# Performance work log

Hardware: AMD Instinct MI355X
Metric: run time of the kernel (lower is better)

Reference implementation:

```python
import jax, jax.numpy as jnp
import numpy as np

DIM = 256
NUM_HEADS = 4
HEAD_DIM = DIM // NUM_HEADS
EPS = 1e-5


def setup_inputs() -> dict:
    key = jax.random.key(0)
    ks = jax.random.split(key, 8)
    B, N, C = 8, 2048, DIM
    s = 0.02
    return {
        "x": jax.random.normal(ks[0], (B, N, C), jnp.float32),
        "qkv_w": jax.random.normal(ks[1], (C, 3 * C), jnp.float32) * s,
        "qkv_b": jnp.zeros((3 * C,), jnp.float32),
        "proj_w": jax.random.normal(ks[2], (C, C), jnp.float32) * s,
        "proj_b": jnp.zeros((C,), jnp.float32),
        "ln1_g": jnp.ones((C,), jnp.float32),
        "ln1_b": jnp.zeros((C,), jnp.float32),
        "ln2_g": jnp.ones((C,), jnp.float32),
        "ln2_b": jnp.zeros((C,), jnp.float32),
        "mlp_w1": jax.random.normal(ks[3], (C, 2 * C), jnp.float32) * s,
        "mlp_b1": jnp.zeros((2 * C,), jnp.float32),
        "mlp_w2": jax.random.normal(ks[4], (2 * C, C), jnp.float32) * s,
        "mlp_b2": jnp.zeros((C,), jnp.float32),
    }


def _layernorm(x, g, b):
    mu = jnp.mean(x, axis=-1, keepdims=True)
    var = jnp.mean(jnp.square(x - mu), axis=-1, keepdims=True)
    return (x - mu) * jax.lax.rsqrt(var + EPS) * g + b


def reference(x, qkv_w, qkv_b, proj_w, proj_b, ln1_g, ln1_b, ln2_g, ln2_b,
              mlp_w1, mlp_b1, mlp_w2, mlp_b2):
    B, N, C = x.shape
    H, D = NUM_HEADS, HEAD_DIM
    shortcut = x
    h = _layernorm(x, ln1_g, ln1_b)
    qkv = (h @ qkv_w + qkv_b).reshape(B, N, 3, H, D)
    q = qkv[:, :, 0].transpose(0, 2, 1, 3)  # [B,H,N,D]
    k = qkv[:, :, 1].transpose(0, 2, 1, 3)
    v = qkv[:, :, 2].transpose(0, 2, 1, 3)
    attn = jnp.einsum('bhnd,bhmd->bhnm', q, k) * (D ** -0.5)
    attn = jax.nn.softmax(attn, axis=-1)  # dropout = identity (eval mode)
    o = jnp.einsum('bhnm,bhmd->bhnd', attn, v)
    o = o.transpose(0, 2, 1, 3).reshape(B, N, C)
    x = o @ proj_w + proj_b + shortcut
    h2 = _layernorm(x, ln2_g, ln2_b)
    mlp = jax.nn.gelu(h2 @ mlp_w1 + mlp_b1, approximate=False) @ mlp_w2 + mlp_b2
    return x + mlp
```

## Files before the change

kernel.cpp:

```cpp
#include <hip/hip_runtime.h>

typedef __bf16 bf16;
typedef __bf16 bf16x8 __attribute__((ext_vector_type(8)));
typedef __bf16 bf16x4 __attribute__((ext_vector_type(4)));
typedef float  f32x4  __attribute__((ext_vector_type(4)));
typedef unsigned u32x2 __attribute__((ext_vector_type(2)));

typedef __attribute__((address_space(1))) const void GASV;
typedef __attribute__((address_space(3))) void LASV;

__device__ __forceinline__ void gload16(const void* g, void* l) {
  __builtin_amdgcn_global_load_lds((GASV*)g, (LASV*)l, 16, 0, 0);
}

constexpr float CEXP = 0.125f * 1.44269504088896340736f;

__global__ __launch_bounds__(256) void prep_fused(const float* __restrict__ qkv_w,
                                                  const float* __restrict__ proj_w,
                                                  const float* __restrict__ w1,
                                                  const float* __restrict__ w2,
                                                  bf16* __restrict__ Wtqkv,
                                                  bf16* __restrict__ WtP,
                                                  bf16* __restrict__ Wt1,
                                                  bf16* __restrict__ Wt2,
                                                  const float* __restrict__ x,
                                                  const float* __restrict__ gam,
                                                  const float* __restrict__ bet,
                                                  bf16* __restrict__ hout) {
  __shared__ float td[32][33];
  const int blk = blockIdx.x;
  const int tid = threadIdx.x;
  if (blk >= 512) {
    const int lane = tid & 63;
    const int w = tid >> 6;
    const size_t row = (size_t)(blk - 512) * 4 + w;
    const float4 v = *(const float4*)(x + row * 256 + lane * 4);
    float s1 = v.x + v.y + v.z + v.w;
    float s2 = v.x * v.x + v.y * v.y + v.z * v.z + v.w * v.w;
#pragma unroll
    for (int m = 1; m < 64; m <<= 1) {
      s1 += __shfl_xor(s1, m);
      s2 += __shfl_xor(s2, m);
    }
    const float mu = s1 * (1.0f / 256.0f);
    const float var = s2 * (1.0f / 256.0f) - mu * mu;
    const float rs = rsqrtf(var + 1e-5f);
    const float4 g4 = *(const float4*)(gam + lane * 4);
    const float4 b4 = *(const float4*)(bet + lane * 4);
    bf16x4 o;
    o[0] = (bf16)((v.x - mu) * rs * g4.x + b4.x);
    o[1] = (bf16)((v.y - mu) * rs * g4.y + b4.y);
    o[2] = (bf16)((v.z - mu) * rs * g4.z + b4.z);
    o[3] = (bf16)((v.w - mu) * rs * g4.w + b4.w);
    *(bf16x4*)(hout + row * 256 + lane * 4) = o;
    return;
  }
  const int t = blk;
  const float* src;
  bf16* dst;
  int Kin, Nin, kt, nt;
  if (t < 192)      { src = qkv_w; dst = Wtqkv; Kin = 256; Nin = 768; kt = t & 7;          nt = t >> 3; }
  else if (t < 256) { src = proj_w; dst = WtP;  Kin = 256; Nin = 256; kt = (t - 192) & 7;  nt = (t - 192) >> 3; }
  else if (t < 384) { src = w1;    dst = Wt1;   Kin = 256; Nin = 512; kt = (t - 256) & 7;  nt = (t - 256) >> 3; }
  else              { src = w2;    dst = Wt2;   Kin = 512; Nin = 256; kt = (t - 384) & 15; nt = (t - 384) >> 4; }
  {
    const int r = tid >> 3, c4 = (tid & 7) << 2;
    const float4 v = *(const float4*)(src + (size_t)(kt * 32 + r) * Nin + nt * 32 + c4);
    td[r][c4 + 0] = v.x; td[r][c4 + 1] = v.y; td[r][c4 + 2] = v.z; td[r][c4 + 3] = v.w;
  }
  __syncthreads();
  {
    const int n = tid >> 3, k4 = (tid & 7) << 2;
    bf16x4 o;
#pragma unroll
    for (int i = 0; i < 4; ++i) o[i] = (bf16)td[k4 + i][n];
    *(bf16x4*)(dst + (size_t)(nt * 32 + n) * Kin + kt * 32 + k4) = o;
  }
}

__global__ __launch_bounds__(256) void ln_fwd(const float* __restrict__ x,
                                              const float* __restrict__ gam,
                                              const float* __restrict__ bet,
                                              bf16* __restrict__ out) {
  const int lane = threadIdx.x & 63;
  const int w = threadIdx.x >> 6;
  const size_t row = (size_t)blockIdx.x * 4 + w;
  const float4 v = *(const float4*)(x + row * 256 + lane * 4);
  float s1 = v.x + v.y + v.z + v.w;
  float s2 = v.x * v.x + v.y * v.y + v.z * v.z + v.w * v.w;
#pragma unroll
  for (int m = 1; m < 64; m <<= 1) {
    s1 += __shfl_xor(s1, m);
    s2 += __shfl_xor(s2, m);
  }
  const float mu = s1 * (1.0f / 256.0f);
  const float var = s2 * (1.0f / 256.0f) - mu * mu;
  const float rs = rsqrtf(var + 1e-5f);
  const float4 g4 = *(const float4*)(gam + lane * 4);
  const float4 b4 = *(const float4*)(bet + lane * 4);
  bf16x4 o;
  o[0] = (bf16)((v.x - mu) * rs * g4.x + b4.x);
  o[1] = (bf16)((v.y - mu) * rs * g4.y + b4.y);
  o[2] = (bf16)((v.z - mu) * rs * g4.z + b4.z);
  o[3] = (bf16)((v.w - mu) * rs * g4.w + b4.w);
  *(bf16x4*)(out + row * 256 + lane * 4) = o;
}

template <int EPI>
__global__ __launch_bounds__(512) void gemm_bt(const bf16* __restrict__ A,
                                               const bf16* __restrict__ Bt,
                                               const float* __restrict__ bias,
                                               const float* __restrict__ res,
                                               void* __restrict__ outp,
                                               int M, int N, int K) {
  __shared__ bf16 Al[2][8192];
  __shared__ bf16 Bl[2][8192];
  const int tid = threadIdx.x;
  const int lane = tid & 63;
  const int W = tid >> 6;
  const int wm = W >> 2, wn = W & 3;
  const int qi = lane & 15, g = lane >> 4;
  const int nbm = M >> 7;
  const int bm = (int)blockIdx.x % nbm;
  const int bn = (int)blockIdx.x / nbm;
  const int m0 = bm << 7, n0 = bn << 7;
  const int nk = K >> 6;

  const char* asrc[2];
  const char* bsrc[2];
#pragma unroll
  for (int p = 0; p < 2; ++p) {
    const int s = p * 8 + W;
    const int row = (s >> 3) * 64 + ((s >> 1) & 3) * 16 + qi;
    const int kb = (s & 1) * 64 + g * 16;
    asrc[p] = (const char*)(A + (size_t)(m0 + row) * K) + kb;
    bsrc[p] = (const char*)(Bt + (size_t)(n0 + row) * K) + kb;
  }

  f32x4 acc[4][2];
#pragma unroll
  for (int i = 0; i < 4; ++i)
#pragma unroll
    for (int j = 0; j < 2; ++j) acc[i][j] = (f32x4){0.f, 0.f, 0.f, 0.f};

  auto stage = [&](int sl) {
#pragma unroll
    for (int p = 0; p < 2; ++p) {
      gload16(asrc[p], (char*)&Al[sl][0] + (p * 8 + W) * 1024);
      gload16(bsrc[p], (char*)&Bl[sl][0] + (p * 8 + W) * 1024);
      asrc[p] += 128;
      bsrc[p] += 128;
    }
  };

  stage(0);
  asm volatile("s_waitcnt vmcnt(0)" ::: "memory");
  __builtin_amdgcn_s_barrier();

  for (int t = 0; t < nk; ++t) {
    if (t + 1 < nk) stage((t + 1) & 1);
    const char* pa = (const char*)&Al[t & 1][0] + wm * 8192 + lane * 16;
    const char* pb = (const char*)&Bl[t & 1][0] + lane * 16;
    bf16x8 av[4][2], bv[2][2];
#pragma unroll
    for (int f = 0; f < 4; ++f)
#pragma unroll
      for (int ks = 0; ks < 2; ++ks)
        av[f][ks] = *(const bf16x8*)(pa + (f * 2 + ks) * 1024);
#pragma unroll
    for (int fn = 0; fn < 2; ++fn)
#pragma unroll
      for (int ks = 0; ks < 2; ++ks) {
        const int r16 = wn * 2 + fn;
        bv[fn][ks] = *(const bf16x8*)(pb + ((r16 >> 2) * 8 + (r16 & 3) * 2 + ks) * 1024);
      }
    __builtin_amdgcn_s_setprio(1);
#pragma unroll
    for (int fm = 0; fm < 4; ++fm)
#pragma unroll
      for (int fn = 0; fn < 2; ++fn) {
        acc[fm][fn] = __builtin_amdgcn_mfma_f32_16x16x32_bf16(av[fm][0], bv[fn][0], acc[fm][fn], 0, 0, 0);
        acc[fm][fn] = __builtin_amdgcn_mfma_f32_16x16x32_bf16(av[fm][1], bv[fn][1], acc[fm][fn], 0, 0, 0);
      }
    __builtin_amdgcn_s_setprio(0);
    asm volatile("s_waitcnt vmcnt(0)" ::: "memory");
    __builtin_amdgcn_s_barrier();
  }

#pragma unroll
  for (int fm = 0; fm < 4; ++fm)
#pragma unroll
    for (int fn = 0; fn < 2; ++fn) {
      const int r0 = m0 + wm * 64 + fm * 16 + g * 4;
      const int c = n0 + wn * 32 + fn * 16 + qi;
#pragma unroll
      for (int j = 0; j < 4; ++j) {
        const int r = r0 + j;
        const float v = acc[fm][fn][j];
        if constexpr (EPI == 0) {
          ((bf16*)outp)[(size_t)r * N + c] = (bf16)(v + bias[c]);
        } else if constexpr (EPI == 1) {
          ((bf16*)outp)[(size_t)r * 2048 + ((size_t)(c >> 11)) * 524288 + (c & 2047)] =
              (bf16)(v + bias[r]);
        } else if constexpr (EPI == 2) {
          ((float*)outp)[(size_t)r * N + c] = v + bias[c] + res[(size_t)r * N + c];
        } else {
          const float u = v + bias[c];
          ((bf16*)outp)[(size_t)r * N + c] = (bf16)(u * 0.5f * (1.0f + erff(u * 0.70710678118f)));
        }
      }
    }
}

__global__ __launch_bounds__(256) void attn_fwd(const bf16* __restrict__ qk,
                                                const bf16* __restrict__ vT,
                                                bf16* __restrict__ po0,
                                                bf16* __restrict__ po1,
                                                float* __restrict__ pstats) {
  __shared__ bf16 Kl[2][4096];
  __shared__ bf16 Vl[2][4096];
  __shared__ bf16 Pl[4][1024];
  const int tid = threadIdx.x;
  const int lane = tid & 63;
  const int w = tid >> 6;
  const int g = lane >> 4;
  const int qi = lane & 15;
  const int bid = (int)blockIdx.x;
  const int bh = bid & 31;
  const int qt = (bid >> 5) & 15;
  const int s = bid >> 9;
  const int b = bh >> 2, h = bh & 3;

  const size_t qrow0 = (size_t)b * 2048 + qt * 128 + w * 32 + qi;
  bf16x8 qf[2][2];
#pragma unroll
  for (int f = 0; f < 2; ++f) {
    const bf16* qp = qk + (qrow0 + f * 16) * 512 + h * 64 + g * 8;
    qf[f][0] = *(const bf16x8*)qp;
    qf[f][1] = *(const bf16x8*)(qp + 32);
  }

  float mrun[2] = {0.f, 0.f};
  float lsum[2] = {0.f, 0.f};
  f32x4 o[4][2];
#pragma unroll
  for (int i = 0; i < 4; ++i)
#pragma unroll
    for (int f = 0; f < 2; ++f) o[i][f] = (f32x4){0.f, 0.f, 0.f, 0.f};

  constexpr float THR = 8.0f / CEXP;

  const char* kbase = (const char*)qk + ((size_t)b * 2048) * 1024 + 512 + h * 128 +
                      (size_t)s * 16 * 65536;
  const char* vbase = (const char*)vT + (size_t)bh * 262144 + (size_t)s * 16 * 128;
  const char* ks[2];
  const char* vs[2];
#pragma unroll
  for (int i = 0; i < 2; ++i) {
    const int fk = i * 2 + (w >> 1);
    const int half = w & 1;
    ks[i] = kbase + (fk * 16 + qi) * 1024 + half * 64 + g * 16;
    vs[i] = vbase + (size_t)(fk * 16 + qi) * 4096 + half * 64 + g * 16;
  }
  char* const pw = (char*)&Pl[w][0];
  int paddrb[2];
#pragma unroll
  for (int bb = 0; bb < 2; ++bb)
    paddrb[bb] = (bb * 2 + (g >> 1)) * 256 + qi * 16 + (g & 1) * 8;
  const char* const prd = pw + lane * 16;

  auto stage = [&](int slot) {
    char* kd = (char*)&Kl[0][0] + slot * 8192 + w * 1024;
    char* vd = (char*)&Vl[0][0] + slot * 8192 + w * 1024;
    gload16(ks[0], kd);
    gload16(ks[1], kd + 4096);
    gload16(vs[0], vd);
    gload16(vs[1], vd + 4096);
    ks[0] += 65536; ks[1] += 65536;
    vs[0] += 128;   vs[1] += 128;
  };

  stage(0);
  asm volatile("s_waitcnt vmcnt(0)" ::: "memory");
  __builtin_amdgcn_s_barrier();

  for (int t = 0; t < 16; ++t) {
    if (t < 15) stage((t + 1) & 1);
    const char* kb = (const char*)&Kl[0][0] + (t & 1) * 8192 + lane * 16;
    f32x4 st[4][2];
    __builtin_amdgcn_s_setprio(1);
#pragma unroll
    for (int fk = 0; fk < 4; ++fk) {
      const bf16x8 k0 = *(const bf16x8*)(kb + fk * 2048);
      const bf16x8 k1 = *(const bf16x8*)(kb + fk * 2048 + 1024);
#pragma unroll
      for (int f = 0; f < 2; ++f) {
        f32x4 z = (f32x4){0.f, 0.f, 0.f, 0.f};
        st[fk][f] = __builtin_amdgcn_mfma_f32_16x16x32_bf16(k0, qf[f][0], z, 0, 0, 0);
        st[fk][f] = __builtin_amdgcn_mfma_f32_16x16x32_bf16(k1, qf[f][1], st[fk][f], 0, 0, 0);
      }
    }
    __builtin_amdgcn_s_setprio(0);
    float pmax[2];
#pragma unroll
    for (int f = 0; f < 2; ++f) {
      float m0 = fmaxf(fmaxf(st[0][f][0], st[0][f][1]), fmaxf(st[0][f][2], st[0][f][3]));
      float m1 = fmaxf(fmaxf(st[1][f][0], st[1][f][1]), fmaxf(st[1][f][2], st[1][f][3]));
      float m2 = fmaxf(fmaxf(st[2][f][0], st[2][f][1]), fmaxf(st[2][f][2], st[2][f][3]));
      float m3 = fmaxf(fmaxf(st[3][f][0], st[3][f][1]), fmaxf(st[3][f][2], st[3][f][3]));
      pmax[f] = fmaxf(fmaxf(m0, m1), fmaxf(m2, m3));
    }
    if (!__all(pmax[0] <= mrun[0] + THR && pmax[1] <= mrun[1] + THR)) {
#pragma unroll
      for (int f = 0; f < 2; ++f) {
        float mt = fmaxf(pmax[f], __shfl_xor(pmax[f], 16));
        mt = fmaxf(mt, __shfl_xor(mt, 32));
        const float mnew = fmaxf(mrun[f], mt);
        const float alpha = exp2f(CEXP * (mrun[f] - mnew));
        lsum[f] *= alpha;
#pragma unroll
        for (int fd = 0; fd < 4; ++fd)
#pragma unroll
          for (int j = 0; j < 4; ++j) o[fd][f][j] *= alpha;
        mrun[f] = mnew;
      }
    }
    unsigned pk[4][2][2];
#pragma unroll
    for (int f = 0; f < 2; ++f) {
      const float negcm = -CEXP * mrun[f];
      float ts = 0.f;
#pragma unroll
      for (int fk = 0; fk < 4; ++fk)
#pragma unroll
        for (int jp = 0; jp < 2; ++jp) {
          const float p0 = exp2f(fmaf(st[fk][f][2 * jp], CEXP, negcm));
          const float p1 = exp2f(fmaf(st[fk][f][2 * jp + 1], CEXP, negcm));
          ts += p0 + p1;
          union { bf16 h2[2]; unsigned u; } cv;
          cv.h2[0] = (bf16)p0;
          cv.h2[1] = (bf16)p1;
          pk[fk][f][jp] = cv.u;
        }
      lsum[f] += ts;
    }
    const char* vb = (const char*)&Vl[0][0] + (t & 1) * 8192 + lane * 16;
#pragma unroll
    for (int ksl = 0; ksl < 2; ++ksl) {
#pragma unroll
      for (int bb = 0; bb < 2; ++bb) {
        const int fk = 2 * ksl + bb;
#pragma unroll
        for (int f = 0; f < 2; ++f) {
          u32x2 pv2;
          pv2[0] = pk[fk][f][0];
          pv2[1] = pk[fk][f][1];
          *(u32x2*)(pw + f * 1024 + paddrb[bb]) = pv2;
        }
      }
      bf16x8 pa[2];
#pragma unroll
      for (int f = 0; f < 2; ++f) pa[f] = *(const bf16x8*)(prd + f * 1024);
      __builtin_amdgcn_s_setprio(1);
#pragma unroll
      for (int fd = 0; fd < 4; ++fd) {
        const bf16x8 vv = *(const bf16x8*)(vb + fd * 2048 + ksl * 1024);
#pragma unroll
        for (int f = 0; f < 2; ++f)
          o[fd][f] = __builtin_amdgcn_mfma_f32_16x16x32_bf16(vv, pa[f], o[fd][f], 0, 0, 0);
      }
      __builtin_amdgcn_s_setprio(0);
    }
    asm volatile("s_waitcnt vmcnt(0)" ::: "memory");
    __builtin_amdgcn_s_barrier();
  }

#pragma unroll
  for (int f = 0; f < 2; ++f) {
    float l = lsum[f];
    l += __shfl_xor(l, 16);
    l += __shfl_xor(l, 32);
    lsum[f] = l;
  }
  if (g == 0) {
#pragma unroll
    for (int f = 0; f < 2; ++f) {
      float2 sv;
      sv.x = mrun[f];
      sv.y = lsum[f];
      *(float2*)(pstats + (((size_t)s * 32 + bh) * 2048 + qt * 128 + w * 32 + f * 16 + qi) * 2) = sv;
    }
  }
  bf16* const pob = s ? po1 : po0;
#pragma unroll
  for (int f = 0; f < 2; ++f) {
    bf16* const orow = pob + (qrow0 + f * 16) * 256 + h * 64 + g * 4;
#pragma unroll
    for (int fd = 0; fd < 4; ++fd) {
      bf16x4 ov;
#pragma unroll
      for (int j = 0; j < 4; ++j) ov[j] = (bf16)o[fd][f][j];
      *(bf16x4*)(orow + fd * 16) = ov;
    }
  }
}

__global__ __launch_bounds__(256) void attn_merge(const bf16* __restrict__ po0,
                                                  const bf16* __restrict__ po1,
                                                  const float* __restrict__ pstats,
                                                  bf16* __restrict__ ob) {
  const int idx = blockIdx.x * 256 + threadIdx.x;
  const int r = idx >> 6;
  const int cq = (idx & 63) * 4;
  const int h = cq >> 6;
  const int bh = (r >> 11) * 4 + h;
  const int ql = r & 2047;
  const float2 s0 = *(const float2*)(pstats + (((size_t)bh) * 2048 + ql) * 2);
  const float2 s1 = *(const float2*)(pstats + (((size_t)32 + bh) * 2048 + ql) * 2);
  const float M = fmaxf(s0.x, s1.x);
  const float a0 = exp2f(CEXP * (s0.x - M));
  const float a1 = exp2f(CEXP * (s1.x - M));
  const float inv = 1.0f / (s0.y * a0 + s1.y * a1);
  const bf16x4 p0 = *(const bf16x4*)(po0 + (size_t)r * 256 + cq);
  const bf16x4 p1 = *(const bf16x4*)(po1 + (size_t)r * 256 + cq);
  bf16x4 ov;
#pragma unroll
  for (int j = 0; j < 4; ++j)
    ov[j] = (bf16)(((float)p0[j] * a0 + (float)p1[j] * a1) * inv);
  *(bf16x4*)(ob + (size_t)r * 256 + cq) = ov;
}

extern "C" void kernel_launch(void* const* d_in, const int* in_sizes, int n_in,
                              void* d_out, int out_size, void* d_ws, size_t ws_size,
                              hipStream_t stream) {
  const float* x      = (const float*)d_in[0];
  const float* qkv_w  = (const float*)d_in[1];
  const float* qkv_b  = (const float*)d_in[2];
  const float* proj_w = (const float*)d_in[3];
  const float* proj_b = (const float*)d_in[4];
  const float* ln1_g  = (const float*)d_in[5];
  const float* ln1_b  = (const float*)d_in[6];
  const float* ln2_g  = (const float*)d_in[7];
  const float* ln2_b  = (const float*)d_in[8];
  const float* mlp_w1 = (const float*)d_in[9];
  const float* mlp_b1 = (const float*)d_in[10];
  const float* mlp_w2 = (const float*)d_in[11];
  const float* mlp_b2 = (const float*)d_in[12];
  float* out = (float*)d_out;

  char* ws = (char*)d_ws;
  bf16* Wtqkv = (bf16*)(ws);
  bf16* WtP   = (bf16*)(ws + 393216);
  bf16* Wt1   = (bf16*)(ws + 524288);
  bf16* Wt2   = (bf16*)(ws + 786432);
  bf16* h     = (bf16*)(ws + 1048576);
  bf16* qkb   = (bf16*)(ws + 9437184);
  bf16* vT    = (bf16*)(ws + 26214400);
  bf16* po1   = (bf16*)(ws + 34603008);
  float* x2   = (float*)(ws + 42991616);
  float* pstats = (float*)(ws + 59768832);
  bf16* po0  = h;
  bf16* obuf = vT;
  bf16* a1 = qkb;
  bf16* h2 = h;

  prep_fused<<<4608, 256, 0, stream>>>(qkv_w, proj_w, mlp_w1, mlp_w2, Wtqkv, WtP, Wt1, Wt2,
                                       x, ln1_g, ln1_b, h);
  gemm_bt<0><<<512, 512, 0, stream>>>(h, Wtqkv, qkv_b, nullptr, qkb, 16384, 512, 256);
  gemm_bt<1><<<256, 512, 0, stream>>>(Wtqkv + 512 * 256, h, qkv_b + 512, nullptr, vT, 256, 16384, 256);
  attn_fwd<<<1024, 256, 0, stream>>>(qkb, vT, po0, po1, pstats);
  attn_merge<<<4096, 256, 0, stream>>>(po0, po1, pstats, obuf);
  gemm_bt<2><<<256, 512, 0, stream>>>(obuf, WtP, proj_b, x, x2, 16384, 256, 256);
  ln_fwd<<<4096, 256, 0, stream>>>(x2, ln2_g, ln2_b, h2);
  gemm_bt<3><<<512, 512, 0, stream>>>(h2, Wt1, mlp_b1, nullptr, a1, 16384, 512, 256);
  gemm_bt<2><<<256, 512, 0, stream>>>(a1, Wt2, mlp_b2, x2, out, 16384, 256, 512);
}
```

Measured before the change: 170.7 us.

## Merge QKV and V-transpose GEMMs into one launch; triple-buffer N=256 GEMMs

The QK and transposed-V projection GEMMs now run in a single 768-block launch that branches on block index. This removes one kernel launch and lets the two GEMMs share the GPU at the same time. The proj and MLP2 GEMMs get a three-stage LDS pipeline that keeps two tiles in flight, waiting with vmcnt(4) instead of draining fully. This hides more global-load latency, at the cost of 96KB of LDS per block, which may lower occupancy.

Result: faster. 161.2 us (-5.6%).

```diff
diff --git a/kernel.cpp b/kernel.cpp
--- a/kernel.cpp
+++ b/kernel.cpp
@@ -106,23 +106,22 @@
   *(bf16x4*)(out + row * 256 + lane * 4) = o;
 }
 
-template <int EPI>
-__global__ __launch_bounds__(512) void gemm_bt(const bf16* __restrict__ A,
-                                               const bf16* __restrict__ Bt,
-                                               const float* __restrict__ bias,
-                                               const float* __restrict__ res,
-                                               void* __restrict__ outp,
-                                               int M, int N, int K) {
-  __shared__ bf16 Al[2][8192];
-  __shared__ bf16 Bl[2][8192];
+template <int EPI, int NB>
+__device__ __forceinline__ void gemm_core(bf16* __restrict__ ldsA, bf16* __restrict__ ldsB,
+                                          const bf16* __restrict__ A,
+                                          const bf16* __restrict__ Bt,
+                                          const float* __restrict__ bias,
+                                          const float* __restrict__ res,
+                                          void* __restrict__ outp,
+                                          int M, int N, int K, int bid) {
   const int tid = threadIdx.x;
   const int lane = tid & 63;
   const int W = tid >> 6;
   const int wm = W >> 2, wn = W & 3;
   const int qi = lane & 15, g = lane >> 4;
   const int nbm = M >> 7;
-  const int bm = (int)blockIdx.x % nbm;
-  const int bn = (int)blockIdx.x / nbm;
+  const int bm = bid % nbm;
+  const int bn = bid / nbm;
   const int m0 = bm << 7, n0 = bn << 7;
   const int nk = K >> 6;
 
@@ -146,21 +145,30 @@
   auto stage = [&](int sl) {
 #pragma unroll
     for (int p = 0; p < 2; ++p) {
-      gload16(asrc[p], (char*)&Al[sl][0] + (p * 8 + W) * 1024);
-      gload16(bsrc[p], (char*)&Bl[sl][0] + (p * 8 + W) * 1024);
+      gload16(asrc[p], (char*)ldsA + sl * 16384 + (p * 8 + W) * 1024);
+      gload16(bsrc[p], (char*)ldsB + sl * 16384 + (p * 8 + W) * 1024);
       asrc[p] += 128;
       bsrc[p] += 128;
     }
   };
 
-  stage(0);
-  asm volatile("s_waitcnt vmcnt(0)" ::: "memory");
+  if constexpr (NB == 2) {
+    stage(0);
+    asm volatile("s_waitcnt vmcnt(0)" ::: "memory");
+  } else {
+    stage(0);
+    stage(1);
+    asm volatile("s_waitcnt vmcnt(4)" ::: "memory");
+  }
   __builtin_amdgcn_s_barrier();
 
+  int cur = 0, nxt = (NB == 2) ? 1 : 2;
   for (int t = 0; t < nk; ++t) {
-    if (t + 1 < nk) stage((t + 1) & 1);
-    const char* pa = (const char*)&Al[t & 1][0] + wm * 8192 + lane * 16;
-    const char* pb = (const char*)&Bl[t & 1][0] + lane * 16;
+    if constexpr (NB == 2) {
+      if (t + 1 < nk) stage(nxt);
+    }
+    const char* pa = (const char*)ldsA + cur * 16384 + wm * 8192 + lane * 16;
+    const char* pb = (const char*)ldsB + cur * 16384 + lane * 16;
     bf16x8 av[4][2], bv[2][2];
 #pragma unroll
     for (int f = 0; f < 4; ++f)
@@ -174,6 +182,9 @@
         const int r16 = wn * 2 + fn;
         bv[fn][ks] = *(const bf16x8*)(pb + ((r16 >> 2) * 8 + (r16 & 3) * 2 + ks) * 1024);
       }
+    if constexpr (NB == 3) {
+      if (t + 2 < nk) stage(nxt);
+    }
     __builtin_amdgcn_s_setprio(1);
 #pragma unroll
     for (int fm = 0; fm < 4; ++fm)
@@ -183,8 +194,18 @@
         acc[fm][fn] = __builtin_amdgcn_mfma_f32_16x16x32_bf16(av[fm][1], bv[fn][1], acc[fm][fn], 0, 0, 0);
       }
     __builtin_amdgcn_s_setprio(0);
-    asm volatile("s_waitcnt vmcnt(0)" ::: "memory");
+    if constexpr (NB == 2) {
+      asm volatile("s_waitcnt vmcnt(0)" ::: "memory");
+    } else {
+      if (t + 2 < nk) {
+        asm volatile("s_waitcnt vmcnt(4)" ::: "memory");
+      } else {
+        asm volatile("s_waitcnt vmcnt(0)" ::: "memory");
+      }
+    }
     __builtin_amdgcn_s_barrier();
+    cur = (cur == NB - 1) ? 0 : cur + 1;
+    nxt = (nxt == NB - 1) ? 0 : nxt + 1;
   }
 
 #pragma unroll
@@ -210,6 +231,34 @@
         }
       }
     }
+}
+
+__global__ __launch_bounds__(512) void gemm_qkv_fused(const bf16* __restrict__ h,
+                                                      const bf16* __restrict__ Wtqkv,
+                                                      const float* __restrict__ qkv_b,
+                                                      bf16* __restrict__ qkb,
+                                                      bf16* __restrict__ vT) {
+  __shared__ bf16 ldsA[2 * 8192];
+  __shared__ bf16 ldsB[2 * 8192];
+  const int bid = (int)blockIdx.x;
+  if (bid < 512) {
+    gemm_core<0, 2>(ldsA, ldsB, h, Wtqkv, qkv_b, nullptr, qkb, 16384, 512, 256, bid);
+  } else {
+    gemm_core<1, 2>(ldsA, ldsB, Wtqkv + 512 * 256, h, qkv_b + 512, nullptr, vT,
+                    256, 16384, 256, bid - 512);
+  }
+}
+
+template <int EPI, int NB>
+__global__ __launch_bounds__(512) void gemm_one(const bf16* __restrict__ A,
+                                                const bf16* __restrict__ Bt,
+                                                const float* __restrict__ bias,
+                                                const float* __restrict__ res,
+                                                void* __restrict__ outp,
+                                                int M, int N, int K) {
+  __shared__ bf16 ldsA[NB * 8192];
+  __shared__ bf16 ldsB[NB * 8192];
+  gemm_core<EPI, NB>(ldsA, ldsB, A, Bt, bias, res, outp, M, N, K, (int)blockIdx.x);
 }
 
 __global__ __launch_bounds__(256) void attn_fwd(const bf16* __restrict__ qk,
@@ -466,12 +515,11 @@
 
   prep_fused<<<4608, 256, 0, stream>>>(qkv_w, proj_w, mlp_w1, mlp_w2, Wtqkv, WtP, Wt1, Wt2,
                                        x, ln1_g, ln1_b, h);
-  gemm_bt<0><<<512, 512, 0, stream>>>(h, Wtqkv, qkv_b, nullptr, qkb, 16384, 512, 256);
-  gemm_bt<1><<<256, 512, 0, stream>>>(Wtqkv + 512 * 256, h, qkv_b + 512, nullptr, vT, 256, 16384, 256);
+  gemm_qkv_fused<<<768, 512, 0, stream>>>(h, Wtqkv, qkv_b, qkb, vT);
   attn_fwd<<<1024, 256, 0, stream>>>(qkb, vT, po0, po1, pstats);
   attn_merge<<<4096, 256, 0, stream>>>(po0, po1, pstats, obuf);
-  gemm_bt<2><<<256, 512, 0, stream>>>(obuf, WtP, proj_b, x, x2, 16384, 256, 256);
+  gemm_one<2, 3><<<256, 512, 0, stream>>>(obuf, WtP, proj_b, x, x2, 16384, 256, 256);
   ln_fwd<<<4096, 256, 0, stream>>>(x2, ln2_g, ln2_b, h2);
-  gemm_bt<3><<<512, 512, 0, stream>>>(h2, Wt1, mlp_b1, nullptr, a1, 16384, 512, 256);
-  gemm_bt<2><<<256, 512, 0, stream>>>(a1, Wt2, mlp_b2, x2, out, 16384, 256, 512);
-}
+  gemm_one<3, 2><<<512, 512, 0, stream>>>(h2, Wt1, mlp_b1, nullptr, a1, 16384, 512, 256);
+  gemm_one<2, 3><<<256, 512, 0, stream>>>(a1, Wt2, mlp_b2, x2, out, 16384, 256, 512);
+}
```
